# Kernel optimization log

Hardware: AMD Instinct MI355X
Metric: run time of the kernel (lower is better)

## Reference

```python
import jax, jax.numpy as jnp
import numpy as np

B, IN, OUT, E = 4096, 256, 256, 16


def setup_inputs() -> dict:
    key = jax.random.key(0)
    k1, k2, k3, k4, k5, k6 = jax.random.split(key, 6)
    return {
        "input": jax.random.normal(k1, (B, IN), dtype=jnp.float32),
        "route_index": jax.random.randint(k2, (B,), 0, E),
        "weight": jax.random.normal(k3, (E, OUT * IN), dtype=jnp.float32) * 0.02,
        "weight_fact": jax.random.normal(k4, (1, OUT * IN), dtype=jnp.float32) * 0.02,
        "bias": jax.random.normal(k5, (E, OUT), dtype=jnp.float32) * 0.02,
        "bias_fact": jax.random.normal(k6, (1, OUT), dtype=jnp.float32) * 0.02,
    }


def reference(input, route_index, weight, weight_fact, bias, bias_fact):
    b = input.shape[0]
    # per-token expert weight gather + shared factorized weight
    expert_weight = (weight[route_index] + weight_fact).reshape(b, OUT, IN)
    expert_bias = bias[route_index] + bias_fact  # [b, OUT]
    # batched matvec
    out = jnp.einsum("bmn,bn->bm", expert_weight, input) + expert_bias
    return out
```

## Files before the change

kernel.cpp:

```cpp
#include <hip/hip_runtime.h>


#define B_TOK 4096
#define IN_F 256
#define OUT_F 256
#define NEXP 16
#define WEL (OUT_F * IN_F)
#define NSB 16

typedef __attribute__((ext_vector_type(8))) short bhalf8;
typedef __attribute__((ext_vector_type(4))) float v4f;

#define WSUM_OFF 0u
#define PART_OFF 2097152u

__device__ __forceinline__ unsigned short f2bf(float f) {
    unsigned u = __float_as_uint(f);
    u += 0x7FFFu + ((u >> 16) & 1u);
    return (unsigned short)(u >> 16);
}

__global__ __launch_bounds__(256) void k_prep(
    const int* __restrict__ ridx, const float* __restrict__ w,
    const float* __restrict__ wf, unsigned short* __restrict__ wsum,
    int* __restrict__ part) {
    int bid = blockIdx.x;
    int tid = threadIdx.x;
    if (bid < 512) {
        int id = (bid * 256 + tid) * 8;
        const float4 a0 = *(const float4*)(w + id);
        const float4 a1 = *(const float4*)(w + id + 4);
        int fo = id & (WEL - 1);
        const float4 f0 = *(const float4*)(wf + fo);
        const float4 f1 = *(const float4*)(wf + fo + 4);
        bhalf8 v;
        v[0] = (short)f2bf(a0.x + f0.x); v[1] = (short)f2bf(a0.y + f0.y);
        v[2] = (short)f2bf(a0.z + f0.z); v[3] = (short)f2bf(a0.w + f0.w);
        v[4] = (short)f2bf(a1.x + f1.x); v[5] = (short)f2bf(a1.y + f1.y);
        v[6] = (short)f2bf(a1.z + f1.z); v[7] = (short)f2bf(a1.w + f1.w);
        *(bhalf8*)(wsum + id) = v;
    } else {
        __shared__ int h[NEXP];
        if (tid < NEXP) h[tid] = 0;
        __syncthreads();
        int sb = bid - 512;
        atomicAdd(&h[ridx[sb * 256 + tid]], 1);
        __syncthreads();
        if (tid < NEXP) part[sb * NEXP + tid] = h[tid];
    }
}

__global__ __launch_bounds__(256) void k_gemm(
    const unsigned short* __restrict__ wsum, const float* __restrict__ x,
    const int* __restrict__ ridx, const int* __restrict__ part,
    const float* __restrict__ bias, const float* __restrict__ bf,
    float* __restrict__ out) {
    __shared__ int pfx[NSB + 1];
    __shared__ int wc[4];
    __shared__ int stk[16];

    int e = blockIdx.y;
    int j = blockIdx.x;
    int tid = threadIdx.x;

    __shared__ int pc[NSB];
    if (tid < NSB) pc[tid] = part[tid * NEXP + e];
    __syncthreads();
    if (tid == 0) {
        int a = 0;
        for (int sb = 0; sb < NSB; ++sb) { pfx[sb] = a; a += pc[sb]; }
        pfx[NSB] = a;
    }
    __syncthreads();
    int cnt = pfx[NSB];
    int start = j * 16;
    if (start >= cnt) return;
    int rem = cnt - start;
    int rows = rem < 16 ? rem : 16;
    int end = start + rows;

    int wave = tid >> 6;
    int lane = tid & 63;

    for (int sb = 0; sb < NSB; ++sb) {
        if (pfx[sb + 1] <= start || pfx[sb] >= end) continue;
        int tok = sb * 256 + tid;
        bool m = (ridx[tok] == e);
        unsigned long long mask = __ballot(m);
        if (lane == 0) wc[wave] = (int)__popcll(mask);
        __syncthreads();
        int wbase = 0;
        for (int wv = 0; wv < wave; ++wv) wbase += wc[wv];
        int rank = wbase + (int)__popcll(mask & ((1ull << lane) - 1ull));
        int slot = pfx[sb] + rank;
        if (m && slot >= start && slot < end) stk[slot - start] = tok;
        __syncthreads();
    }
    if (tid < 16 && tid >= rows) stk[tid] = stk[0];
    __syncthreads();

    int l15 = lane & 15;
    int quad = lane >> 4;

    const float* xrow = x + stk[l15] * IN_F + quad * 8;
    const unsigned short* wbase_p =
        wsum + e * WEL + (wave * 64 + l15) * IN_F + quad * 8;

    v4f acc[4];
    #pragma unroll
    for (int n = 0; n < 4; ++n) acc[n] = (v4f){0.f, 0.f, 0.f, 0.f};

    #pragma unroll
    for (int ks = 0; ks < 8; ++ks) {
        const float4 a0 = *(const float4*)(xrow + ks * 32);
        const float4 a1 = *(const float4*)(xrow + ks * 32 + 4);
        bhalf8 a;
        a[0] = (short)f2bf(a0.x); a[1] = (short)f2bf(a0.y);
        a[2] = (short)f2bf(a0.z); a[3] = (short)f2bf(a0.w);
        a[4] = (short)f2bf(a1.x); a[5] = (short)f2bf(a1.y);
        a[6] = (short)f2bf(a1.z); a[7] = (short)f2bf(a1.w);
        bhalf8 b0 = *(const bhalf8*)(wbase_p + 0 * 16 * IN_F + ks * 32);
        bhalf8 b1 = *(const bhalf8*)(wbase_p + 1 * 16 * IN_F + ks * 32);
        bhalf8 b2 = *(const bhalf8*)(wbase_p + 2 * 16 * IN_F + ks * 32);
        bhalf8 b3 = *(const bhalf8*)(wbase_p + 3 * 16 * IN_F + ks * 32);
        acc[0] = __builtin_amdgcn_mfma_f32_16x16x32_bf16(a, b0, acc[0], 0, 0, 0);
        acc[1] = __builtin_amdgcn_mfma_f32_16x16x32_bf16(a, b1, acc[1], 0, 0, 0);
        acc[2] = __builtin_amdgcn_mfma_f32_16x16x32_bf16(a, b2, acc[2], 0, 0, 0);
        acc[3] = __builtin_amdgcn_mfma_f32_16x16x32_bf16(a, b3, acc[3], 0, 0, 0);
    }

    #pragma unroll
    for (int n = 0; n < 4; ++n) {
        int m = wave * 64 + n * 16 + l15;
        float bb = bias[e * OUT_F + m] + bf[m];
        #pragma unroll
        for (int r = 0; r < 4; ++r) {
            int row = quad * 4 + r;
            if (row < rows) out[stk[row] * OUT_F + m] = acc[n][r] + bb;
        }
    }
}

extern "C" void kernel_launch(void* const* d_in, const int* in_sizes, int n_in,
                              void* d_out, int out_size, void* d_ws, size_t ws_size,
                              hipStream_t stream) {
    const float* x = (const float*)d_in[0];
    const int* ridx = (const int*)d_in[1];
    const float* w = (const float*)d_in[2];
    const float* wf = (const float*)d_in[3];
    const float* bias = (const float*)d_in[4];
    const float* bf = (const float*)d_in[5];
    float* out = (float*)d_out;
    char* ws = (char*)d_ws;

    unsigned short* wsum = (unsigned short*)(ws + WSUM_OFF);
    int* part = (int*)(ws + PART_OFF);

    k_prep<<<528, 256, 0, stream>>>(ridx, w, wf, wsum, part);
    k_gemm<<<dim3(32, NEXP), 256, 0, stream>>>(wsum, x, ridx, part, bias, bf, out);
}
```

Measured before the change: 84.00 us.

## Fuse weight prep and routing histogram into single grouped GEMM kernel

Drops the separate prep kernel that converted expert weights plus shared factor to bf16 and built per-block routing histograms. The fused kernel has each block count its expert's tokens directly from route_index, then reads fp32 expert weights and the shared factor, adds and converts them to bf16 inline before the MFMA. This removes one launch and the write and re-read of a bf16 weight copy. In exchange every token-tile block re-reads its expert's fp32 weights and the factor, and the grid is reordered so blocks of the same expert are no longer adjacent, which may reduce L2 reuse.

```diff
diff --git a/kernel.cpp b/kernel.cpp
--- a/kernel.cpp
+++ b/kernel.cpp
@@ -11,76 +11,63 @@
 typedef __attribute__((ext_vector_type(8))) short bhalf8;
 typedef __attribute__((ext_vector_type(4))) float v4f;
 
-#define WSUM_OFF 0u
-#define PART_OFF 2097152u
-
 __device__ __forceinline__ unsigned short f2bf(float f) {
     unsigned u = __float_as_uint(f);
     u += 0x7FFFu + ((u >> 16) & 1u);
     return (unsigned short)(u >> 16);
 }
 
-__global__ __launch_bounds__(256) void k_prep(
-    const int* __restrict__ ridx, const float* __restrict__ w,
-    const float* __restrict__ wf, unsigned short* __restrict__ wsum,
-    int* __restrict__ part) {
-    int bid = blockIdx.x;
-    int tid = threadIdx.x;
-    if (bid < 512) {
-        int id = (bid * 256 + tid) * 8;
-        const float4 a0 = *(const float4*)(w + id);
-        const float4 a1 = *(const float4*)(w + id + 4);
-        int fo = id & (WEL - 1);
-        const float4 f0 = *(const float4*)(wf + fo);
-        const float4 f1 = *(const float4*)(wf + fo + 4);
-        bhalf8 v;
-        v[0] = (short)f2bf(a0.x + f0.x); v[1] = (short)f2bf(a0.y + f0.y);
-        v[2] = (short)f2bf(a0.z + f0.z); v[3] = (short)f2bf(a0.w + f0.w);
-        v[4] = (short)f2bf(a1.x + f1.x); v[5] = (short)f2bf(a1.y + f1.y);
-        v[6] = (short)f2bf(a1.z + f1.z); v[7] = (short)f2bf(a1.w + f1.w);
-        *(bhalf8*)(wsum + id) = v;
-    } else {
-        __shared__ int h[NEXP];
-        if (tid < NEXP) h[tid] = 0;
-        __syncthreads();
-        int sb = bid - 512;
-        atomicAdd(&h[ridx[sb * 256 + tid]], 1);
-        __syncthreads();
-        if (tid < NEXP) part[sb * NEXP + tid] = h[tid];
-    }
+__device__ __forceinline__ bhalf8 cvt8(float4 a0, float4 a1) {
+    bhalf8 v;
+    v[0] = (short)f2bf(a0.x); v[1] = (short)f2bf(a0.y);
+    v[2] = (short)f2bf(a0.z); v[3] = (short)f2bf(a0.w);
+    v[4] = (short)f2bf(a1.x); v[5] = (short)f2bf(a1.y);
+    v[6] = (short)f2bf(a1.z); v[7] = (short)f2bf(a1.w);
+    return v;
 }
 
-__global__ __launch_bounds__(256) void k_gemm(
-    const unsigned short* __restrict__ wsum, const float* __restrict__ x,
-    const int* __restrict__ ridx, const int* __restrict__ part,
-    const float* __restrict__ bias, const float* __restrict__ bf,
+__global__ __launch_bounds__(256) void k_fused(
+    const float* __restrict__ x, const int* __restrict__ ridx,
+    const float* __restrict__ w, const float* __restrict__ wf,
+    const float* __restrict__ bias, const float* __restrict__ bfv,
     float* __restrict__ out) {
     __shared__ int pfx[NSB + 1];
+    __shared__ int pcs[NSB];
     __shared__ int wc[4];
     __shared__ int stk[16];
 
-    int e = blockIdx.y;
-    int j = blockIdx.x;
+    int e = blockIdx.x;
+    int j = blockIdx.y;
     int tid = threadIdx.x;
+    int wave = tid >> 6;
+    int lane = tid & 63;
 
-    __shared__ int pc[NSB];
-    if (tid < NSB) pc[tid] = part[tid * NEXP + e];
+    {
+        int c = 0;
+        const int4* rp = (const int4*)(ridx + tid * 16);
+        #pragma unroll
+        for (int i = 0; i < 4; ++i) {
+            int4 v = rp[i];
+            c += (v.x == e) + (v.y == e) + (v.z == e) + (v.w == e);
+        }
+        #pragma unroll
+        for (int s = 1; s < 16; s <<= 1) c += __shfl_xor(c, s);
+        if ((tid & 15) == 0) pcs[tid >> 4] = c;
+    }
     __syncthreads();
     if (tid == 0) {
         int a = 0;
-        for (int sb = 0; sb < NSB; ++sb) { pfx[sb] = a; a += pc[sb]; }
+        for (int sb = 0; sb < NSB; ++sb) { pfx[sb] = a; a += pcs[sb]; }
         pfx[NSB] = a;
     }
     __syncthreads();
+
     int cnt = pfx[NSB];
     int start = j * 16;
     if (start >= cnt) return;
     int rem = cnt - start;
     int rows = rem < 16 ? rem : 16;
     int end = start + rows;
-
-    int wave = tid >> 6;
-    int lane = tid & 63;
 
     for (int sb = 0; sb < NSB; ++sb) {
         if (pfx[sb + 1] <= start || pfx[sb] >= end) continue;
@@ -103,8 +90,8 @@
     int quad = lane >> 4;
 
     const float* xrow = x + stk[l15] * IN_F + quad * 8;
-    const unsigned short* wbase_p =
-        wsum + e * WEL + (wave * 64 + l15) * IN_F + quad * 8;
+    const float* wrow = w + e * WEL + (wave * 64 + l15) * IN_F + quad * 8;
+    const float* frow = wf + (wave * 64 + l15) * IN_F + quad * 8;
 
     v4f acc[4];
     #pragma unroll
@@ -114,25 +101,28 @@
     for (int ks = 0; ks < 8; ++ks) {
         const float4 a0 = *(const float4*)(xrow + ks * 32);
         const float4 a1 = *(const float4*)(xrow + ks * 32 + 4);
-        bhalf8 a;
-        a[0] = (short)f2bf(a0.x); a[1] = (short)f2bf(a0.y);
-        a[2] = (short)f2bf(a0.z); a[3] = (short)f2bf(a0.w);
-        a[4] = (short)f2bf(a1.x); a[5] = (short)f2bf(a1.y);
-        a[6] = (short)f2bf(a1.z); a[7] = (short)f2bf(a1.w);
-        bhalf8 b0 = *(const bhalf8*)(wbase_p + 0 * 16 * IN_F + ks * 32);
-        bhalf8 b1 = *(const bhalf8*)(wbase_p + 1 * 16 * IN_F + ks * 32);
-        bhalf8 b2 = *(const bhalf8*)(wbase_p + 2 * 16 * IN_F + ks * 32);
-        bhalf8 b3 = *(const bhalf8*)(wbase_p + 3 * 16 * IN_F + ks * 32);
-        acc[0] = __builtin_amdgcn_mfma_f32_16x16x32_bf16(a, b0, acc[0], 0, 0, 0);
-        acc[1] = __builtin_amdgcn_mfma_f32_16x16x32_bf16(a, b1, acc[1], 0, 0, 0);
-        acc[2] = __builtin_amdgcn_mfma_f32_16x16x32_bf16(a, b2, acc[2], 0, 0, 0);
-        acc[3] = __builtin_amdgcn_mfma_f32_16x16x32_bf16(a, b3, acc[3], 0, 0, 0);
+        bhalf8 a = cvt8(a0, a1);
+        #pragma unroll
+        for (int n = 0; n < 4; ++n) {
+            const float* wp = wrow + n * (16 * IN_F) + ks * 32;
+            const float* fp = frow + n * (16 * IN_F) + ks * 32;
+            const float4 b0 = *(const float4*)(wp);
+            const float4 b1 = *(const float4*)(wp + 4);
+            const float4 g0 = *(const float4*)(fp);
+            const float4 g1 = *(const float4*)(fp + 4);
+            float4 s0 = make_float4(b0.x + g0.x, b0.y + g0.y,
+                                    b0.z + g0.z, b0.w + g0.w);
+            float4 s1 = make_float4(b1.x + g1.x, b1.y + g1.y,
+                                    b1.z + g1.z, b1.w + g1.w);
+            bhalf8 b = cvt8(s0, s1);
+            acc[n] = __builtin_amdgcn_mfma_f32_16x16x32_bf16(a, b, acc[n], 0, 0, 0);
+        }
     }
 
     #pragma unroll
     for (int n = 0; n < 4; ++n) {
         int m = wave * 64 + n * 16 + l15;
-        float bb = bias[e * OUT_F + m] + bf[m];
+        float bb = bias[e * OUT_F + m] + bfv[m];
         #pragma unroll
         for (int r = 0; r < 4; ++r) {
             int row = quad * 4 + r;
@@ -144,6 +134,7 @@
 extern "C" void kernel_launch(void* const* d_in, const int* in_sizes, int n_in,
                               void* d_out, int out_size, void* d_ws, size_t ws_size,
                               hipStream_t stream) {
+    (void)in_sizes; (void)n_in; (void)out_size; (void)d_ws; (void)ws_size;
     const float* x = (const float*)d_in[0];
     const int* ridx = (const int*)d_in[1];
     const float* w = (const float*)d_in[2];
@@ -151,11 +142,6 @@
     const float* bias = (const float*)d_in[4];
     const float* bf = (const float*)d_in[5];
     float* out = (float*)d_out;
-    char* ws = (char*)d_ws;
 
-    unsigned short* wsum = (unsigned short*)(ws + WSUM_OFF);
-    int* part = (int*)(ws + PART_OFF);
-
-    k_prep<<<528, 256, 0, stream>>>(ridx, w, wf, wsum, part);
-    k_gemm<<<dim3(32, NEXP), 256, 0, stream>>>(wsum, x, ridx, part, bias, bf, out);
+    k_fused<<<dim3(NEXP, 32), 256, 0, stream>>>(x, ridx, w, wf, bias, bf, out);
 }
```

Measured after the change: 101.4 us. 20.8% more time.
